# Kernel optimization log

Hardware: AMD Instinct MI355X
Metric: run time of the kernel (lower is better)

## Reference

```python
import jax, jax.numpy as jnp
import numpy as np

B, L, D, H = 2, 2048, 1024, 16
HD = D // H  # head_dim = 64


def setup_inputs() -> dict:
    key = jax.random.key(0)
    ks = jax.random.split(key, 10)
    s_in = 1.0 / np.sqrt(D)
    x = jax.random.normal(ks[0], (B, L, D), dtype=jnp.float32)
    attn_mask = jnp.ones((B, L), dtype=jnp.int32)
    # Per-head QKV projections stacked along head axis: (H, D, HD)
    Wq = jax.random.normal(ks[1], (H, D, HD), dtype=jnp.float32) * s_in
    bq = jnp.zeros((H, HD), dtype=jnp.float32)
    Wk = jax.random.normal(ks[2], (H, D, HD), dtype=jnp.float32) * s_in
    bk = jnp.zeros((H, HD), dtype=jnp.float32)
    Wv = jax.random.normal(ks[3], (H, D, HD), dtype=jnp.float32) * s_in
    bv = jnp.zeros((H, HD), dtype=jnp.float32)
    # Output projection (D, D)
    Wo = jax.random.normal(ks[4], (D, D), dtype=jnp.float32) * s_in
    bo = jnp.zeros((D,), dtype=jnp.float32)
    return {"x": x, "attn_mask": attn_mask, "Wq": Wq, "bq": bq,
            "Wk": Wk, "bk": bk, "Wv": Wv, "bv": bv, "Wo": Wo, "bo": bo}


def reference(x, attn_mask, Wq, bq, Wk, bk, Wv, bv, Wo, bo):
    # Batched equivalent of the per-head loop: q,k,v -> (B, H, L, HD)
    q = jnp.einsum('bld,hde->bhle', x, Wq) + bq[None, :, None, :]
    k = jnp.einsum('bld,hde->bhle', x, Wk) + bk[None, :, None, :]
    v = jnp.einsum('bld,hde->bhle', x, Wv) + bv[None, :, None, :]
    scale = 1.0 / jnp.sqrt(jnp.asarray(HD, dtype=x.dtype))
    scores = jnp.einsum('bhle,bhme->bhlm', q, k) * scale  # (B, H, L, L)
    # attn_mask (B, L): mask out keys where mask == 0
    neg = jnp.asarray(-1e9, dtype=scores.dtype)
    scores = jnp.where(attn_mask[:, None, None, :] != 0, scores, neg)
    attn = jax.nn.softmax(scores, axis=-1)
    ctx = jnp.einsum('bhlm,bhme->bhle', attn, v)  # (B, H, L, HD)
    # Concatenate heads (head h occupies dims [h*HD:(h+1)*HD]) then project
    concat = jnp.transpose(ctx, (0, 2, 1, 3)).reshape(B, L, D)
    out = jnp.einsum('bld,de->ble', concat, Wo) + bo
    return out
```

## Files before the change

kernel.cpp:

```cpp
#include <hip/hip_runtime.h>

constexpr int Bz = 2, Lz = 2048, Dz = 1024, Hz = 16, HDz = 64;
constexpr int QSZ = Bz * Hz * Lz * HDz;

typedef __attribute__((ext_vector_type(8))) __bf16 bf16x8;
typedef __attribute__((ext_vector_type(4))) float f32x4;

__device__ __forceinline__ unsigned short f2b(float x) {
    union { float f; unsigned int u; } c; c.f = x;
    unsigned int u = c.u;
    return (unsigned short)((u + 0x7fffu + ((u >> 16) & 1u)) >> 16);
}
__device__ __forceinline__ void ld8(const float* p, float* f) {
    float4 a = *(const float4*)p, b = *(const float4*)(p + 4);
    f[0] = a.x; f[1] = a.y; f[2] = a.z; f[3] = a.w;
    f[4] = b.x; f[5] = b.y; f[6] = b.z; f[7] = b.w;
}
__device__ __forceinline__ int swb(int row, int e) {
    return row * 64 + ((((e >> 3) ^ row) & 7) << 3) + (e & 7);
}

__global__ void ws_sentinel(float* __restrict__ out) {
    if (threadIdx.x == 0 && blockIdx.x == 0) out[0] = 100.0f;
}

__global__ __launch_bounds__(256) void cvt_x(
    const float* __restrict__ x, unsigned short* __restrict__ xb) {
    int idx = (blockIdx.x * 256 + threadIdx.x) * 8;
    float f[8]; ld8(x + idx, f);
    union { unsigned short s[8]; uint4 u; } o;
    #pragma unroll
    for (int j = 0; j < 8; ++j) o.s[j] = f2b(f[j]);
    *(uint4*)(xb + idx) = o.u;
}

__global__ __launch_bounds__(256) void cvt_w(
    const float* __restrict__ Wq, const float* __restrict__ Wk,
    const float* __restrict__ Wv, const float* __restrict__ Wo,
    unsigned short* __restrict__ Wt, unsigned short* __restrict__ Wot) {
    const int tid = threadIdx.x;
    const int z = blockIdx.z;
    const int kseg = blockIdx.x * 4 + (tid >> 6);
    const int k0 = kseg * 16;
    unsigned short o[16];
    if (z < 3) {
        const float* W = (z == 0) ? Wq : (z == 1) ? Wk : Wv;
        const int h = blockIdx.y, n = tid & 63;
        const float* src = W + (size_t)h * Dz * HDz;
        #pragma unroll
        for (int j = 0; j < 16; ++j) o[j] = f2b(src[(size_t)(k0 + j) * HDz + n]);
        unsigned short* dst = Wt + ((size_t)((z * Hz + h) * HDz) + n) * Dz + k0;
        *(uint4*)dst = *(uint4*)o;
        *(uint4*)(dst + 8) = *(uint4*)(o + 8);
    } else {
        const int n = blockIdx.y * 64 + (tid & 63);
        #pragma unroll
        for (int j = 0; j < 16; ++j) o[j] = f2b(Wo[(size_t)(k0 + j) * Dz + n]);
        unsigned short* dst = Wot + (size_t)n * Dz + k0;
        *(uint4*)dst = *(uint4*)o;
        *(uint4*)(dst + 8) = *(uint4*)(o + 8);
    }
}

__global__ __launch_bounds__(256) void qkv_mfma(
    const unsigned short* __restrict__ xb, const unsigned short* __restrict__ Wt,
    const float* __restrict__ bq, const float* __restrict__ bk,
    const float* __restrict__ bv, unsigned short* __restrict__ qkv) {
    const int l0 = blockIdx.x * 256;
    const int h = blockIdx.y;
    const int which = blockIdx.z % 3;
    const int b = blockIdx.z / 3;
    const float* bias = (which == 0) ? bq : (which == 1) ? bk : bv;
    const int tid = threadIdx.x, wave = tid >> 6, lane = tid & 63;
    const int quad = lane >> 4, l16 = lane & 15;

    __shared__ __align__(16) unsigned short As[256 * 64];
    __shared__ __align__(16) unsigned short Bs[64 * 64];

    const unsigned short* xrow = xb + (size_t)(b * Lz + l0) * Dz;
    const unsigned short* wbase = Wt + (size_t)((which * Hz + h) * HDz) * Dz;

    f32x4 acc[4][4];
    #pragma unroll
    for (int mi = 0; mi < 4; ++mi)
        #pragma unroll
        for (int ni = 0; ni < 4; ++ni) acc[mi][ni] = (f32x4){0.f, 0.f, 0.f, 0.f};

    for (int t = 0; t < Dz / 64; ++t) {
        const int k0 = t * 64;
        #pragma unroll
        for (int i = 0; i < 8; ++i) {
            int ci = tid + i * 256;
            int row = ci >> 3, c = ci & 7;
            uint4 u = *(const uint4*)(xrow + (size_t)row * Dz + k0 + c * 8);
            *(uint4*)&As[row * 64 + ((c ^ (row & 7)) << 3)] = u;
        }
        #pragma unroll
        for (int i = 0; i < 2; ++i) {
            int ci = tid + i * 256;
            int n = ci >> 3, c = ci & 7;
            uint4 u = *(const uint4*)(wbase + (size_t)n * Dz + k0 + c * 8);
            *(uint4*)&Bs[n * 64 + ((c ^ (n & 7)) << 3)] = u;
        }
        __syncthreads();
        #pragma unroll
        for (int kh = 0; kh < 2; ++kh) {
            bf16x8 a[4], bb[4];
            #pragma unroll
            for (int mi = 0; mi < 4; ++mi)
                a[mi] = *(const bf16x8*)&As[swb(wave * 64 + mi * 16 + l16, kh * 32 + quad * 8)];
            #pragma unroll
            for (int ni = 0; ni < 4; ++ni)
                bb[ni] = *(const bf16x8*)&Bs[swb(ni * 16 + l16, kh * 32 + quad * 8)];
            #pragma unroll
            for (int mi = 0; mi < 4; ++mi)
                #pragma unroll
                for (int ni = 0; ni < 4; ++ni)
                    acc[mi][ni] = __builtin_amdgcn_mfma_f32_16x16x32_bf16(
                        a[mi], bb[ni], acc[mi][ni], 0, 0, 0);
        }
        __syncthreads();
    }
    unsigned short* outp = qkv + (size_t)which * QSZ + ((size_t)(b * Hz + h) * Lz + l0) * HDz;
    #pragma unroll
    for (int ni = 0; ni < 4; ++ni) {
        float bvv = bias[h * HDz + ni * 16 + l16];
        #pragma unroll
        for (int mi = 0; mi < 4; ++mi)
            #pragma unroll
            for (int r = 0; r < 4; ++r) {
                int row = wave * 64 + mi * 16 + quad * 4 + r;
                outp[(size_t)row * HDz + ni * 16 + l16] = f2b(acc[mi][ni][r] + bvv);
            }
    }
}

__global__ __launch_bounds__(256) void attn_mfma(
    unsigned short* __restrict__ qkv, const int* __restrict__ mask) {
    const int b = blockIdx.z, h = blockIdx.y, qb = blockIdx.x;
    const int wave = threadIdx.x >> 6, lane = threadIdx.x & 63;
    const int quad = lane >> 4, l16 = lane & 15;
    unsigned short* Q = qkv + (size_t)((b * Hz + h) * Lz) * HDz;
    const unsigned short* K = Q + QSZ;
    const unsigned short* V = Q + 2 * (size_t)QSZ;

    __shared__ __align__(16) unsigned short Ks[64 * 64];
    __shared__ __align__(16) unsigned short Vt[64 * 64];
    __shared__ __align__(16) unsigned short Pw[4][32 * 64];

    const int row0 = qb * 128 + wave * 32;
    bf16x8 aq[2][2];
    #pragma unroll
    for (int s = 0; s < 2; ++s) {
        const unsigned short* qp = Q + (size_t)(row0 + s * 16 + l16) * HDz;
        aq[s][0] = *(const bf16x8*)(qp + quad * 8);
        aq[s][1] = *(const bf16x8*)(qp + 32 + quad * 8);
    }

    f32x4 O[2][4];
    #pragma unroll
    for (int s = 0; s < 2; ++s)
        #pragma unroll
        for (int nc = 0; nc < 4; ++nc) O[s][nc] = (f32x4){0.f, 0.f, 0.f, 0.f};
    float lacc[2] = {0.f, 0.f};

    const int vp = threadIdx.x & 31, vc = threadIdx.x >> 5;

    for (int t = 0; t < Lz / 64; ++t) {
        const int kt0 = t * 64;
        #pragma unroll
        for (int i = 0; i < 2; ++i) {
            int ci = threadIdx.x + i * 256;
            int key = ci >> 3, c = ci & 7;
            uint4 u = *(const uint4*)(K + (size_t)(kt0 + key) * HDz + c * 8);
            *(uint4*)&Ks[key * 64 + ((c ^ (key & 7)) << 3)] = u;
        }
        {
            const unsigned short* vsrc = V + (size_t)(kt0 + 2 * vp) * HDz + vc * 8;
            uint4 u0 = *(const uint4*)vsrc;
            uint4 u1 = *(const uint4*)(vsrc + HDz);
            unsigned short a0[8], a1[8];
            *(uint4*)a0 = u0; *(uint4*)a1 = u1;
            unsigned int* Vt32 = (unsigned int*)Vt;
            #pragma unroll
            for (int j = 0; j < 8; ++j) {
                int row = vc * 8 + j;
                Vt32[row * 32 + ((((vp >> 2) ^ (row & 7)) << 2) + (vp & 3))] =
                    (unsigned int)a0[j] | ((unsigned int)a1[j] << 16);
            }
        }
        unsigned long long bal = __ballot(mask[b * Lz + kt0 + lane] != 0);
        bool allv = (bal == ~0ull);
        __syncthreads();

        float sh[4][4];
        if (allv) {
            #pragma unroll
            for (int kc = 0; kc < 4; ++kc)
                #pragma unroll
                for (int r = 0; r < 4; ++r) sh[kc][r] = -12.0f;
        } else {
            #pragma unroll
            for (int kc = 0; kc < 4; ++kc)
                #pragma unroll
                for (int r = 0; r < 4; ++r)
                    sh[kc][r] = mask[b * Lz + kt0 + kc * 16 + quad * 4 + r] ? -12.0f : -1e9f;
        }

        unsigned short* Pme = Pw[wave];
        #pragma unroll
        for (int kc = 0; kc < 4; ++kc) {
            bf16x8 aK0 = *(const bf16x8*)&Ks[swb(kc * 16 + l16, quad * 8)];
            bf16x8 aK1 = *(const bf16x8*)&Ks[swb(kc * 16 + l16, 32 + quad * 8)];
            #pragma unroll
            for (int s = 0; s < 2; ++s) {
                f32x4 sv = (f32x4){0.f, 0.f, 0.f, 0.f};
                sv = __builtin_amdgcn_mfma_f32_16x16x32_bf16(aK0, aq[s][0], sv, 0, 0, 0);
                sv = __builtin_amdgcn_mfma_f32_16x16x32_bf16(aK1, aq[s][1], sv, 0, 0, 0);
                float p[4];
                #pragma unroll
                for (int r = 0; r < 4; ++r)
                    p[r] = __expf(fmaf(sv[r], 0.125f, sh[kc][r]));
                lacc[s] += (p[0] + p[1]) + (p[2] + p[3]);
                uint2 pk;
                pk.x = (unsigned int)f2b(p[0]) | ((unsigned int)f2b(p[1]) << 16);
                pk.y = (unsigned int)f2b(p[2]) | ((unsigned int)f2b(p[3]) << 16);
                *(uint2*)&Pme[swb(s * 16 + l16, kc * 16 + quad * 4)] = pk;
            }
        }
        #pragma unroll
        for (int kc2 = 0; kc2 < 2; ++kc2) {
            bf16x8 aP0 = *(const bf16x8*)&Pme[swb(l16, kc2 * 32 + quad * 8)];
            bf16x8 aP1 = *(const bf16x8*)&Pme[swb(16 + l16, kc2 * 32 + quad * 8)];
            #pragma unroll
            for (int nc = 0; nc < 4; ++nc) {
                bf16x8 bV = *(const bf16x8*)&Vt[swb(nc * 16 + l16, kc2 * 32 + quad * 8)];
                O[0][nc] = __builtin_amdgcn_mfma_f32_16x16x32_bf16(aP0, bV, O[0][nc], 0, 0, 0);
                O[1][nc] = __builtin_amdgcn_mfma_f32_16x16x32_bf16(aP1, bV, O[1][nc], 0, 0, 0);
            }
        }
        __syncthreads();
    }
    float inv[2];
    #pragma unroll
    for (int s = 0; s < 2; ++s) {
        lacc[s] += __shfl_xor(lacc[s], 16, 64);
        lacc[s] += __shfl_xor(lacc[s], 32, 64);
        inv[s] = 1.0f / lacc[s];
    }
    #pragma unroll
    for (int s = 0; s < 2; ++s)
        #pragma unroll
        for (int r = 0; r < 4; ++r) {
            float invr = __shfl(inv[s], quad * 4 + r, 64);
            int row = row0 + s * 16 + quad * 4 + r;
            #pragma unroll
            for (int nc = 0; nc < 4; ++nc)
                Q[(size_t)row * HDz + nc * 16 + l16] = f2b(O[s][nc][r] * invr);
        }
}

__global__ __launch_bounds__(256) void out_mfma(
    const unsigned short* __restrict__ ctx, const unsigned short* __restrict__ Wot,
    const float* __restrict__ bo, float* __restrict__ out) {
    const int r0 = blockIdx.x * 128;
    const int n0 = blockIdx.y * 64;
    const int b = r0 >> 11, lbase = r0 & 2047;
    const int tid = threadIdx.x, wave = tid >> 6, lane = tid & 63;
    const int quad = lane >> 4, l16 = lane & 15;

    __shared__ __align__(16) unsigned short As[128 * 64];
    __shared__ __align__(16) unsigned short Bs[64 * 64];

    f32x4 acc[2][4];
    #pragma unroll
    for (int mi = 0; mi < 2; ++mi)
        #pragma unroll
        for (int ni = 0; ni < 4; ++ni) acc[mi][ni] = (f32x4){0.f, 0.f, 0.f, 0.f};

    for (int t = 0; t < Hz; ++t) {
        const unsigned short* abase = ctx + ((size_t)(b * Hz + t) * Lz + lbase) * HDz;
        #pragma unroll
        for (int i = 0; i < 4; ++i) {
            int ci = tid + i * 256;
            int row = ci >> 3, c = ci & 7;
            uint4 u = *(const uint4*)(abase + (size_t)row * HDz + c * 8);
            *(uint4*)&As[row * 64 + ((c ^ (row & 7)) << 3)] = u;
        }
        #pragma unroll
        for (int i = 0; i < 2; ++i) {
            int ci = tid + i * 256;
            int n = ci >> 3, c = ci & 7;
            uint4 u = *(const uint4*)(Wot + (size_t)(n0 + n) * Dz + t * 64 + c * 8);
            *(uint4*)&Bs[n * 64 + ((c ^ (n & 7)) << 3)] = u;
        }
        __syncthreads();
        #pragma unroll
        for (int kh = 0; kh < 2; ++kh) {
            bf16x8 a[2], bb[4];
            #pragma unroll
            for (int mi = 0; mi < 2; ++mi)
                a[mi] = *(const bf16x8*)&As[swb(wave * 32 + mi * 16 + l16, kh * 32 + quad * 8)];
            #pragma unroll
            for (int ni = 0; ni < 4; ++ni)
                bb[ni] = *(const bf16x8*)&Bs[swb(ni * 16 + l16, kh * 32 + quad * 8)];
            #pragma unroll
            for (int mi = 0; mi < 2; ++mi)
                #pragma unroll
                for (int ni = 0; ni < 4; ++ni)
                    acc[mi][ni] = __builtin_amdgcn_mfma_f32_16x16x32_bf16(
                        a[mi], bb[ni], acc[mi][ni], 0, 0, 0);
        }
        __syncthreads();
    }
    #pragma unroll
    for (int ni = 0; ni < 4; ++ni) {
        float bvv = bo[n0 + ni * 16 + l16];
        #pragma unroll
        for (int mi = 0; mi < 2; ++mi)
            #pragma unroll
            for (int r = 0; r < 4; ++r) {
                int row = r0 + wave * 32 + mi * 16 + quad * 4 + r;
                out[(size_t)row * Dz + n0 + ni * 16 + l16] = acc[mi][ni][r] + bvv;
            }
    }
}

extern "C" void kernel_launch(void* const* d_in, const int* in_sizes, int n_in,
                              void* d_out, int out_size, void* d_ws, size_t ws_size,
                              hipStream_t stream) {
    const float* x    = (const float*)d_in[0];
    const int*   mask = (const int*)d_in[1];
    const float* Wq = (const float*)d_in[2];
    const float* bq = (const float*)d_in[3];
    const float* Wk = (const float*)d_in[4];
    const float* bk = (const float*)d_in[5];
    const float* Wv = (const float*)d_in[6];
    const float* bv = (const float*)d_in[7];
    const float* Wo = (const float*)d_in[8];
    const float* bo = (const float*)d_in[9];
    float* out = (float*)d_out;

    const size_t WT_E  = (size_t)3 * Hz * HDz * Dz;
    const size_t WOT_E = (size_t)Dz * Dz;
    const size_t NEED = 256 + ((size_t)3 * QSZ + WT_E + WOT_E) * sizeof(unsigned short);
    if (ws_size < NEED) {
        ws_sentinel<<<1, 64, 0, stream>>>(out);
        return;
    }
    unsigned short* qkv = (unsigned short*)((char*)d_ws + 256);
    unsigned short* Wt  = qkv + (size_t)3 * QSZ;
    unsigned short* Wot = Wt + WT_E;
    unsigned short* xb  = (unsigned short*)d_out;

    cvt_x<<<(Bz * Lz * Dz) / (256 * 8), 256, 0, stream>>>(x, xb);
    cvt_w<<<dim3(16, 16, 4), 256, 0, stream>>>(Wq, Wk, Wv, Wo, Wt, Wot);
    qkv_mfma<<<dim3(Lz / 256, Hz, Bz * 3), 256, 0, stream>>>(xb, Wt, bq, bk, bv, qkv);
    attn_mfma<<<dim3(Lz / 128, Hz, Bz), 256, 0, stream>>>(qkv, mask);
    out_mfma<<<dim3((Bz * Lz) / 128, Dz / 64), 256, 0, stream>>>(qkv, Wot, bo, out);
}
```

Baseline: 248.7 us.

## Split attention over key range into two partial passes plus a combine kernel

Each attention block now processes only half of the keys, which doubles the grid along the batch axis to give more blocks per CU. Unnormalized partial outputs are written in bf16 to scratch space in the output buffer. Row sums are accumulated into a zeroed workspace with atomics. A new combine kernel adds the two partials, normalizes them and writes the context, at the cost of an extra memset, an extra kernel launch, extra memory traffic and an additional bf16 rounding of the partials.

```diff
diff --git a/kernel.cpp b/kernel.cpp
--- a/kernel.cpp
+++ b/kernel.cpp
@@ -2,10 +2,15 @@
 
 constexpr int Bz = 2, Lz = 2048, Dz = 1024, Hz = 16, HDz = 64;
 constexpr int QSZ = Bz * Hz * Lz * HDz;
+constexpr int SPLIT = 2;
+constexpr int KSPAN = Lz / SPLIT;
 
 typedef __attribute__((ext_vector_type(8))) __bf16 bf16x8;
 typedef __attribute__((ext_vector_type(4))) float f32x4;
 
+__device__ __forceinline__ float b2f(unsigned int u) {
+    union { float f; unsigned int i; } c; c.i = u << 16; return c.f;
+}
 __device__ __forceinline__ unsigned short f2b(float x) {
     union { float f; unsigned int u; } c; c.f = x;
     unsigned int u = c.u;
@@ -136,11 +141,13 @@
 }
 
 __global__ __launch_bounds__(256) void attn_mfma(
-    unsigned short* __restrict__ qkv, const int* __restrict__ mask) {
-    const int b = blockIdx.z, h = blockIdx.y, qb = blockIdx.x;
+    const unsigned short* __restrict__ qkv, const int* __restrict__ mask,
+    unsigned short* __restrict__ Opart, float* __restrict__ lsb) {
+    const int b = blockIdx.z >> 1, split = blockIdx.z & 1;
+    const int h = blockIdx.y, qb = blockIdx.x;
     const int wave = threadIdx.x >> 6, lane = threadIdx.x & 63;
     const int quad = lane >> 4, l16 = lane & 15;
-    unsigned short* Q = qkv + (size_t)((b * Hz + h) * Lz) * HDz;
+    const unsigned short* Q = qkv + (size_t)((b * Hz + h) * Lz) * HDz;
     const unsigned short* K = Q + QSZ;
     const unsigned short* V = Q + 2 * (size_t)QSZ;
 
@@ -166,8 +173,8 @@
 
     const int vp = threadIdx.x & 31, vc = threadIdx.x >> 5;
 
-    for (int t = 0; t < Lz / 64; ++t) {
-        const int kt0 = t * 64;
+    for (int t = 0; t < KSPAN / 64; ++t) {
+        const int kt0 = split * KSPAN + t * 64;
         #pragma unroll
         for (int i = 0; i < 2; ++i) {
             int ci = threadIdx.x + i * 256;
@@ -241,23 +248,42 @@
         }
         __syncthreads();
     }
-    float inv[2];
     #pragma unroll
     for (int s = 0; s < 2; ++s) {
         lacc[s] += __shfl_xor(lacc[s], 16, 64);
         lacc[s] += __shfl_xor(lacc[s], 32, 64);
-        inv[s] = 1.0f / lacc[s];
-    }
+    }
+    const size_t rowbase = (size_t)(b * Hz + h) * Lz + row0;
+    if (quad == 0) {
+        atomicAdd(&lsb[rowbase + l16], lacc[0]);
+        atomicAdd(&lsb[rowbase + 16 + l16], lacc[1]);
+    }
+    unsigned short* Os = Opart + (size_t)split * QSZ + rowbase * HDz - (size_t)row0 * HDz
+                         + (size_t)row0 * HDz;
     #pragma unroll
     for (int s = 0; s < 2; ++s)
         #pragma unroll
         for (int r = 0; r < 4; ++r) {
-            float invr = __shfl(inv[s], quad * 4 + r, 64);
-            int row = row0 + s * 16 + quad * 4 + r;
+            int row = s * 16 + quad * 4 + r;
             #pragma unroll
             for (int nc = 0; nc < 4; ++nc)
-                Q[(size_t)row * HDz + nc * 16 + l16] = f2b(O[s][nc][r] * invr);
-        }
+                Os[(size_t)row * HDz + nc * 16 + l16] = f2b(O[s][nc][r]);
+        }
+}
+
+__global__ __launch_bounds__(256) void combine(
+    const unsigned short* __restrict__ Opart, const float* __restrict__ lsb,
+    unsigned short* __restrict__ ctx) {
+    int idx8 = (blockIdx.x * 256 + threadIdx.x) * 8;
+    float inv = 1.0f / lsb[idx8 >> 6];
+    uint4 u0 = *(const uint4*)(Opart + idx8);
+    uint4 u1 = *(const uint4*)(Opart + QSZ + idx8);
+    unsigned short a0[8], a1[8], o[8];
+    *(uint4*)a0 = u0; *(uint4*)a1 = u1;
+    #pragma unroll
+    for (int j = 0; j < 8; ++j)
+        o[j] = f2b((b2f(a0[j]) + b2f(a1[j])) * inv);
+    *(uint4*)(ctx + idx8) = *(uint4*)o;
 }
 
 __global__ __launch_bounds__(256) void out_mfma(
@@ -343,7 +369,9 @@
 
     const size_t WT_E  = (size_t)3 * Hz * HDz * Dz;
     const size_t WOT_E = (size_t)Dz * Dz;
-    const size_t NEED = 256 + ((size_t)3 * QSZ + WT_E + WOT_E) * sizeof(unsigned short);
+    const size_t LS_E  = (size_t)Bz * Hz * Lz;
+    const size_t NEED = 256 + ((size_t)3 * QSZ + WT_E + WOT_E) * sizeof(unsigned short)
+                        + LS_E * sizeof(float);
     if (ws_size < NEED) {
         ws_sentinel<<<1, 64, 0, stream>>>(out);
         return;
@@ -351,11 +379,15 @@
     unsigned short* qkv = (unsigned short*)((char*)d_ws + 256);
     unsigned short* Wt  = qkv + (size_t)3 * QSZ;
     unsigned short* Wot = Wt + WT_E;
-    unsigned short* xb  = (unsigned short*)d_out;
-
+    float* lsb = (float*)(Wot + WOT_E);
+    unsigned short* xb    = (unsigned short*)d_out;
+    unsigned short* Opart = (unsigned short*)d_out;
+
+    hipMemsetAsync(lsb, 0, LS_E * sizeof(float), stream);
     cvt_x<<<(Bz * Lz * Dz) / (256 * 8), 256, 0, stream>>>(x, xb);
     cvt_w<<<dim3(16, 16, 4), 256, 0, stream>>>(Wq, Wk, Wv, Wo, Wt, Wot);
     qkv_mfma<<<dim3(Lz / 256, Hz, Bz * 3), 256, 0, stream>>>(xb, Wt, bq, bk, bv, qkv);
-    attn_mfma<<<dim3(Lz / 128, Hz, Bz), 256, 0, stream>>>(qkv, mask);
+    attn_mfma<<<dim3(Lz / 128, Hz, Bz * SPLIT), 256, 0, stream>>>(qkv, mask, Opart, lsb);
+    combine<<<QSZ / (256 * 8), 256, 0, stream>>>(Opart, lsb, qkv);
     out_mfma<<<dim3((Bz * Lz) / 128, Dz / 64), 256, 0, stream>>>(qkv, Wot, bo, out);
 }
```

Measured after the change: 230.0 us. -7.5%, faster.
